# Kernel optimization log

Hardware: AMD Instinct MI355X
Metric: run time of the kernel (lower is better)

The kernel has to match this reference:

```python
import jax, jax.numpy as jnp
import numpy as np

N_NODES = 50000
N_EDGES = 800000
N_GRAPHS = 100
IN_DIM = 100
OUT_DIM = 128
N_ETYPES = 4
N_STEPS = 8


def setup_inputs() -> dict:
    key = jax.random.key(0)
    ks = jax.random.split(key, 16)
    s = 0.05
    return {
        "features": jax.random.normal(ks[0], (N_NODES, IN_DIM), jnp.float32),
        "edge_src": jax.random.randint(ks[1], (N_EDGES,), 0, N_NODES, jnp.int32),
        "edge_dst": jax.random.randint(ks[2], (N_EDGES,), 0, N_NODES, jnp.int32),
        "edge_types": jax.random.randint(ks[3], (N_EDGES,), 0, N_ETYPES, jnp.int32),
        "graph_ids": jnp.sort(jax.random.randint(ks[4], (N_NODES,), 0, N_GRAPHS, jnp.int32)),
        "W_msg": jax.random.normal(ks[5], (N_ETYPES, OUT_DIM, OUT_DIM), jnp.float32) * s,
        "b_msg": jax.random.normal(ks[6], (N_ETYPES, OUT_DIM), jnp.float32) * s,
        "W_ih": jax.random.normal(ks[7], (3 * OUT_DIM, OUT_DIM), jnp.float32) * s,
        "W_hh": jax.random.normal(ks[8], (3 * OUT_DIM, OUT_DIM), jnp.float32) * s,
        "b_ih": jax.random.normal(ks[9], (3 * OUT_DIM,), jnp.float32) * s,
        "b_hh": jax.random.normal(ks[10], (3 * OUT_DIM,), jnp.float32) * s,
        "W1": jax.random.normal(ks[11], (256, OUT_DIM), jnp.float32) * s,
        "b1": jax.random.normal(ks[12], (256,), jnp.float32) * s,
        "W2": jax.random.normal(ks[13], (1, 256), jnp.float32) * s,
        "b2": jax.random.normal(ks[14], (1,), jnp.float32) * s,
    }


def _gru_cell(x, h, W_ih, W_hh, b_ih, b_hh):
    # torch.nn.GRUCell: gate order (reset, update, new)
    gi = x @ W_ih.T + b_ih  # [N, 3D]
    gh = h @ W_hh.T + b_hh
    i_r, i_z, i_n = jnp.split(gi, 3, axis=-1)
    h_r, h_z, h_n = jnp.split(gh, 3, axis=-1)
    r = jax.nn.sigmoid(i_r + h_r)
    z = jax.nn.sigmoid(i_z + h_z)
    n = jnp.tanh(i_n + r * h_n)
    return (1.0 - z) * n + z * h


def reference(features, edge_src, edge_dst, edge_types, graph_ids,
              W_msg, b_msg, W_ih, W_hh, b_ih, b_hh, W1, b1, W2, b2):
    n_nodes = features.shape[0]
    # DGL GatedGraphConv: zero-pad input features to out_feats
    h = jnp.pad(features, ((0, 0), (0, OUT_DIM - features.shape[1])))
    for _ in range(N_STEPS):
        # per-edge-type linear transform of source features: [T, N, D]
        transformed = jnp.einsum('nd,tdf->tnf', h, W_msg) + b_msg[:, None, :]
        msgs = transformed[edge_types, edge_src]  # [E, D] gather
        a = jax.ops.segment_sum(msgs, edge_dst, num_segments=n_nodes)  # scatter-add
        h = _gru_cell(a, h, W_ih, W_hh, b_ih, b_hh)
    # masked mean pooling per graph (mask_mean over de-batchified graphs)
    counts = jax.ops.segment_sum(jnp.ones((n_nodes,), h.dtype), graph_ids,
                                 num_segments=N_GRAPHS)
    sums = jax.ops.segment_sum(h, graph_ids, num_segments=N_GRAPHS)
    pooled = sums / jnp.maximum(counts, 1.0)[:, None]  # [B, D]
    # classifier: Linear -> relu -> (dropout: eval noop) -> Linear -> sigmoid
    hidden = jax.nn.relu(pooled @ W1.T + b1)
    logits = hidden @ W2.T + b2  # [B, 1]
    return jax.nn.sigmoid(logits).squeeze(-1)  # [B]
```

## Files before the change

kernel.cpp:

```cpp
#include <hip/hip_runtime.h>
#include <hip/hip_bf16.h>
#include <math.h>

#define N_NODES 50000
#define M_PAD   50048
#define N_EDGES 800000
#define N_GRAPHS 100
#define IN_DIM 100
#define D 128
#define N_STEPS 8
#define NBINS (N_NODES * 4)
#define SCAN_BLOCKS 196

typedef unsigned short ushort_t;
typedef __bf16 bf16x8 __attribute__((ext_vector_type(8)));
typedef float f32x4 __attribute__((ext_vector_type(4)));

__device__ inline ushort_t f2b(float f) {
  __hip_bfloat16 b = __float2bfloat16(f);
  return *reinterpret_cast<ushort_t*>(&b);
}
__device__ inline float b2f(unsigned int u16) {
  unsigned int x = u16 << 16;
  return __builtin_bit_cast(float, x);
}

__device__ __attribute__((always_inline)) inline void gld16(const ushort_t* g, ushort_t* l) {
  __builtin_amdgcn_global_load_lds(
      (const __attribute__((address_space(1))) void*)g,
      (__attribute__((address_space(3))) void*)l, 16, 0, 0);
}

__global__ void pad_cast_kernel(const float* __restrict__ feat, ushort_t* __restrict__ ah) {
  int idx = blockIdx.x * blockDim.x + threadIdx.x;
  if (idx >= N_NODES * D) return;
  int n = idx >> 7, d = idx & 127;
  float v = (d < IN_DIM) ? feat[n * IN_DIM + d] : 0.0f;
  ah[(size_t)n * 256 + 128 + d] = f2b(v);
}

__global__ void prep_bts(const float* __restrict__ W_msg, ushort_t* __restrict__ BtS) {
  int idx = blockIdx.x * blockDim.x + threadIdx.x;
  if (idx >= 128 * 512) return;
  int f = idx >> 9, kp = idx & 511;
  int t = kp >> 7, k = kp & 127;
  BtS[(size_t)f * 512 + kp] = f2b(W_msg[((size_t)t * 128 + k) * 128 + f]);
}

__global__ void prep_wg(const float* __restrict__ W_ih, const float* __restrict__ W_hh,
                        const float* __restrict__ b_ih, const float* __restrict__ b_hh,
                        ushort_t* __restrict__ WgT, float* __restrict__ gbias) {
  int idx = blockIdx.x * blockDim.x + threadIdx.x;
  if (idx >= 512 * 256) return;
  int colp = idx >> 8, k = idx & 255;
  int g = colp >> 6, gate = (colp >> 4) & 3, r = colp & 15;
  int d = g * 16 + r;
  float v;
  if (gate == 3)      v = (k < 128) ? 0.f : W_hh[(size_t)(256 + d) * 128 + (k - 128)];
  else if (gate == 2) v = (k < 128) ? W_ih[(size_t)(256 + d) * 128 + k] : 0.f;
  else {
    int j0 = (gate == 0) ? d : 128 + d;
    v = (k < 128) ? W_ih[(size_t)j0 * 128 + k] : W_hh[(size_t)j0 * 128 + (k - 128)];
  }
  WgT[(size_t)colp * 256 + k] = f2b(v);
  if (k == 0) {
    float bb = (gate == 0) ? b_ih[d] + b_hh[d]
             : (gate == 1) ? b_ih[128 + d] + b_hh[128 + d]
             : (gate == 2) ? b_ih[256 + d] : b_hh[256 + d];
    gbias[colp] = bb;
  }
}

__global__ void hist_kernel(const int* __restrict__ edst, const int* __restrict__ etype,
                            int* __restrict__ cnt2, int* __restrict__ rank) {
  int e = blockIdx.x * 256 + threadIdx.x;
  if (e >= N_EDGES) return;
  rank[e] = atomicAdd(&cnt2[edst[e] * 4 + etype[e]], 1);
}

__global__ __launch_bounds__(1024) void scanA(const int* __restrict__ cnt2,
                                              int* __restrict__ tmp, int* __restrict__ bsum) {
  __shared__ int wsum[16];
  int b = blockIdx.x, t = threadIdx.x;
  int i = b * 1024 + t;
  int lane = t & 63, wid = t >> 6;
  int x = (i < NBINS) ? cnt2[i] : 0;
  #pragma unroll
  for (int s = 1; s < 64; s <<= 1) {
    int y = __shfl_up(x, s, 64);
    if (lane >= s) x += y;
  }
  if (lane == 63) wsum[wid] = x;
  __syncthreads();
  if (wid == 0) {
    int w = (lane < 16) ? wsum[lane] : 0;
    #pragma unroll
    for (int s = 1; s < 16; s <<= 1) {
      int y = __shfl_up(w, s, 64);
      if (lane >= s) w += y;
    }
    if (lane < 16) wsum[lane] = w;
  }
  __syncthreads();
  int wb = (wid > 0) ? wsum[wid - 1] : 0;
  tmp[i] = wb + x;
  if (t == 1023) bsum[b] = wsum[15];
}

__global__ __launch_bounds__(64) void scanB(const int* __restrict__ bsum,
                                            int* __restrict__ bpre) {
  int lane = threadIdx.x;
  int carry = 0;
  for (int base = 0; base < SCAN_BLOCKS; base += 64) {
    int idx = base + lane;
    int v = (idx < SCAN_BLOCKS) ? bsum[idx] : 0;
    int x = v;
    #pragma unroll
    for (int s = 1; s < 64; s <<= 1) {
      int y = __shfl_up(x, s, 64);
      if (lane >= s) x += y;
    }
    if (idx < SCAN_BLOCKS) bpre[idx] = carry + x - v;
    carry += __shfl(x, 63, 64);
  }
}

__global__ __launch_bounds__(1024) void scanC(const int* __restrict__ tmp,
                                              const int* __restrict__ bpre,
                                              int* __restrict__ offs2) {
  int b = blockIdx.x, t = threadIdx.x;
  int i = b * 1024 + t;
  if (i < NBINS) offs2[i + 1] = tmp[i] + bpre[b];
  if (i == 0) offs2[0] = 0;
}

__global__ void fill_kernel(const int* __restrict__ esrc, const int* __restrict__ edst,
                            const int* __restrict__ etype, const int* __restrict__ offs2,
                            const int* __restrict__ rank, int* __restrict__ payload) {
  int e = blockIdx.x * 256 + threadIdx.x;
  if (e >= N_EDGES) return;
  int key = edst[e] * 4 + etype[e];
  payload[offs2[key] + rank[e]] = esrc[e];
}

__global__ __launch_bounds__(256) void gather_kernel(const int* __restrict__ offs2,
    const int* __restrict__ payload, const ushort_t* __restrict__ hb,
    ushort_t* __restrict__ S, float* __restrict__ cntf) {
  int n = blockIdx.x * 4 + (threadIdx.x >> 6);
  int lane = threadIdx.x & 63;
  if (n >= N_NODES) return;
  int bb[5];
  #pragma unroll
  for (int k = 0; k < 5; ++k) bb[k] = offs2[n * 4 + k];
  float a[4][2] = {{0.f, 0.f}, {0.f, 0.f}, {0.f, 0.f}, {0.f, 0.f}};
  const ushort_t* hrow = hb + 128 + lane * 2;
  for (int base = bb[0]; base < bb[4]; base += 64) {
    int lim = min(bb[4], base + 64);
    int cnt = lim - base;
    int pe = (lane < cnt) ? payload[base + lane] : 0;
    #pragma unroll
    for (int t = 0; t < 4; ++t) {
      int lo = max(bb[t], base), hi = min(bb[t + 1], lim);
      int i = lo;
      for (; i + 4 <= hi; i += 4) {
        int s0 = __shfl(pe, i - base, 64);
        int s1 = __shfl(pe, i + 1 - base, 64);
        int s2 = __shfl(pe, i + 2 - base, 64);
        int s3 = __shfl(pe, i + 3 - base, 64);
        unsigned int u0 = *(const unsigned int*)(hrow + (size_t)s0 * 256);
        unsigned int u1 = *(const unsigned int*)(hrow + (size_t)s1 * 256);
        unsigned int u2 = *(const unsigned int*)(hrow + (size_t)s2 * 256);
        unsigned int u3 = *(const unsigned int*)(hrow + (size_t)s3 * 256);
        a[t][0] += b2f(u0 & 0xffff) + b2f(u1 & 0xffff) + b2f(u2 & 0xffff) + b2f(u3 & 0xffff);
        a[t][1] += b2f(u0 >> 16) + b2f(u1 >> 16) + b2f(u2 >> 16) + b2f(u3 >> 16);
      }
      for (; i < hi; ++i) {
        int s0 = __shfl(pe, i - base, 64);
        unsigned int u0 = *(const unsigned int*)(hrow + (size_t)s0 * 256);
        a[t][0] += b2f(u0 & 0xffff);
        a[t][1] += b2f(u0 >> 16);
      }
    }
  }
  #pragma unroll
  for (int t = 0; t < 4; ++t) {
    unsigned int packed = (unsigned int)f2b(a[t][0]) | ((unsigned int)f2b(a[t][1]) << 16);
    *(unsigned int*)(S + (size_t)n * 512 + t * 128 + lane * 2) = packed;
    if (lane == 0) cntf[n * 4 + t] = (float)(bb[t + 1] - bb[t]);
  }
}

template <int MODE, int K>
__global__ __launch_bounds__(256) void mfma_gemm(
    const ushort_t* __restrict__ A, int lda,
    const ushort_t* __restrict__ Bt,
    const float* __restrict__ bias, const float* __restrict__ b_msg,
    const float* __restrict__ cntf,
    ushort_t* __restrict__ ah_out) {
  constexpr int NT  = K / 32;
  constexpr int PRE = 3;
  constexpr int SLOT = 12288;
  __shared__ __align__(16) unsigned char smem[SLOT * 4];
  const int m0 = blockIdx.x * 64, n0 = blockIdx.y * 128;
  int tid = threadIdx.x;
  int wave = tid >> 6, lane = tid & 63;
  int wm = (wave & 1) * 32, wn = (wave >> 1) * 64;
  int quad = lane >> 4, l16 = lane & 15;

  int sr = lane >> 2, sc = lane & 3;
  const ushort_t* gA  = A  + (size_t)(m0 + wave * 16 + sr) * lda + sc * 8;
  const ushort_t* gB0 = Bt + (size_t)(n0 + wave * 32 + sr) * K   + sc * 8;
  const ushort_t* gB1 = gB0 + (size_t)16 * K;

  auto stage = [&](int slot, int t) {
    ushort_t* base = (ushort_t*)(smem + slot * SLOT);
    int k0 = t * 32;
    gld16(gA + k0,  base + wave * 512);
    gld16(gB0 + k0, base + 2048 + wave * 1024);
    gld16(gB1 + k0, base + 2048 + wave * 1024 + 512);
  };

  f32x4 acc[2][4];
  #pragma unroll
  for (int i = 0; i < 2; ++i)
    #pragma unroll
    for (int j = 0; j < 4; ++j) acc[i][j] = (f32x4){0.f, 0.f, 0.f, 0.f};

  #pragma unroll
  for (int t = 0; t < PRE; ++t) stage(t, t);

  #pragma unroll
  for (int t = 0; t < NT; ++t) {
    int infl = NT - 1 - t;
    if (infl >= 2)      asm volatile("s_waitcnt vmcnt(6) lgkmcnt(0)" ::: "memory");
    else if (infl == 1) asm volatile("s_waitcnt vmcnt(3) lgkmcnt(0)" ::: "memory");
    else                asm volatile("s_waitcnt vmcnt(0) lgkmcnt(0)" ::: "memory");
    __builtin_amdgcn_s_barrier();
    if (t + PRE < NT) stage((t + PRE) & 3, t + PRE);
    const ushort_t* As = (const ushort_t*)(smem + (t & 3) * SLOT);
    const ushort_t* Bs = As + 2048;
    bf16x8 af[2], bfr[4];
    #pragma unroll
    for (int i = 0; i < 2; ++i) af[i] = *(const bf16x8*)&As[(wm + i * 16 + l16) * 32 + quad * 8];
    #pragma unroll
    for (int j = 0; j < 4; ++j) bfr[j] = *(const bf16x8*)&Bs[(wn + j * 16 + l16) * 32 + quad * 8];
    #pragma unroll
    for (int i = 0; i < 2; ++i)
      #pragma unroll
      for (int j = 0; j < 4; ++j)
        acc[i][j] = __builtin_amdgcn_mfma_f32_16x16x32_bf16(af[i], bfr[j], acc[i][j], 0, 0, 0);
  }

  if (MODE == 2) {
    ushort_t* Ep = (ushort_t*)smem;
    float bm[4][4];
    #pragma unroll
    for (int j = 0; j < 4; ++j)
      #pragma unroll
      for (int t = 0; t < 4; ++t)
        bm[j][t] = b_msg[t * 128 + wn + j * 16 + l16];
    #pragma unroll
    for (int p = 0; p < 2; ++p) {
      if (p) __syncthreads();
      #pragma unroll
      for (int reg = 0; reg < 4; ++reg) {
        int slot = (wm >> 5) * 16 + quad * 4 + reg;
        int m = m0 + wm + p * 16 + quad * 4 + reg;
        float4 c = *(const float4*)(cntf + (size_t)m * 4);
        #pragma unroll
        for (int j = 0; j < 4; ++j) {
          float val = acc[p][j][reg] + c.x * bm[j][0] + c.y * bm[j][1]
                                     + c.z * bm[j][2] + c.w * bm[j][3];
          Ep[slot * 136 + wn + j * 16 + l16] = f2b(val);
        }
      }
      __syncthreads();
      #pragma unroll
      for (int c2 = 0; c2 < 2; ++c2) {
        int chunk = tid + 256 * c2;
        int slot = chunk >> 4, sub = chunk & 15;
        int m = m0 + (slot & 15) + (slot >> 4) * 32 + p * 16;
        *(uint4*)(ah_out + (size_t)m * 256 + sub * 8) =
            *(const uint4*)&Ep[slot * 136 + sub * 8];
      }
    }
  } else {
    ushort_t* Ap = (ushort_t*)smem;
    int db = (n0 >> 6) * 16;
    int dim_loc = (wn >> 6) * 16 + l16;
    float br = bias[n0 + wn + l16];
    float bz = bias[n0 + wn + 16 + l16];
    float bi = bias[n0 + wn + 32 + l16];
    float bh = bias[n0 + wn + 48 + l16];
    #pragma unroll
    for (int i = 0; i < 2; ++i)
      #pragma unroll
      for (int reg = 0; reg < 4; ++reg) {
        int r_loc = wm + i * 16 + quad * 4 + reg;
        int m = m0 + r_loc;
        float pr  = acc[i][0][reg] + br;
        float pz  = acc[i][1][reg] + bz;
        float in_ = acc[i][2][reg] + bi;
        float hn  = acc[i][3][reg] + bh;
        float r = 1.0f / (1.0f + expf(-pr));
        float z = 1.0f / (1.0f + expf(-pz));
        float nn = tanhf(in_ + r * hn);
        float hold = b2f(A[(size_t)m * lda + 128 + db + dim_loc]);
        float hv = (1.0f - z) * nn + z * hold;
        Ap[r_loc * 40 + dim_loc] = f2b(hv);
      }
    __syncthreads();
    {
      int row = tid >> 2, sub = tid & 3;
      *(uint4*)(ah_out + (size_t)(m0 + row) * 256 + 128 + db + sub * 8) =
          *(const uint4*)&Ap[row * 40 + sub * 8];
    }
  }
}

__global__ __launch_bounds__(128) void pool_kernel(const ushort_t* __restrict__ ah,
    const int* __restrict__ gids, float* __restrict__ pooled, float* __restrict__ gcnt) {
  __shared__ int lo_s, hi_s;
  int g = blockIdx.x, c = blockIdx.y, d = threadIdx.x;
  if (d == 0) {
    int lo = 0, hi = N_NODES;
    while (lo < hi) { int mid = (lo + hi) >> 1; if (gids[mid] < g) lo = mid + 1; else hi = mid; }
    lo_s = lo;
    int lo2 = lo, hi2 = N_NODES;
    while (lo2 < hi2) { int mid = (lo2 + hi2) >> 1; if (gids[mid] < g + 1) lo2 = mid + 1; else hi2 = mid; }
    hi_s = lo2;
  }
  __syncthreads();
  int lo = lo_s, hi = hi_s;
  int len = hi - lo;
  int b = lo + (int)(((long long)len * c) >> 3);
  int e = lo + (int)(((long long)len * (c + 1)) >> 3);
  float s = 0.f;
  for (int n = b; n < e; ++n) s += b2f(ah[(size_t)n * 256 + 128 + d]);
  if (e > b) atomicAdd(&pooled[g * 128 + d], s);
  if (c == 0 && d == 0) gcnt[g] = (float)len;
}

__global__ __launch_bounds__(256) void classifier_kernel(
    const float* __restrict__ pooled, const float* __restrict__ gcnt,
    const float* __restrict__ W1, const float* __restrict__ b1,
    const float* __restrict__ W2, const float* __restrict__ b2,
    float* __restrict__ out) {
  __shared__ float p[D];
  __shared__ float hid[256];
  __shared__ float wsum[4];
  int g = blockIdx.x;
  int t = threadIdx.x;
  float cnt = fmaxf(gcnt[g], 1.0f);
  if (t < D) p[t] = pooled[g * D + t] / cnt;
  __syncthreads();
  float acc = b1[t];
  const float* w = W1 + (size_t)t * D;
  for (int k = 0; k < D; ++k) acc += p[k] * w[k];
  hid[t] = fmaxf(acc, 0.0f);
  __syncthreads();
  float v = hid[t] * W2[t];
  for (int off = 32; off > 0; off >>= 1) v += __shfl_down(v, off, 64);
  if ((t & 63) == 0) wsum[t >> 6] = v;
  __syncthreads();
  if (t == 0) {
    float s = wsum[0] + wsum[1] + wsum[2] + wsum[3] + b2[0];
    out[g] = 1.0f / (1.0f + expf(-s));
  }
}

extern "C" void kernel_launch(void* const* d_in, const int* in_sizes, int n_in,
                              void* d_out, int out_size, void* d_ws, size_t ws_size,
                              hipStream_t stream) {
  const float* features = (const float*)d_in[0];
  const int* esrc  = (const int*)d_in[1];
  const int* edst  = (const int*)d_in[2];
  const int* etype = (const int*)d_in[3];
  const int* gids  = (const int*)d_in[4];
  const float* W_msg = (const float*)d_in[5];
  const float* b_msg = (const float*)d_in[6];
  const float* W_ih  = (const float*)d_in[7];
  const float* W_hh  = (const float*)d_in[8];
  const float* b_ih  = (const float*)d_in[9];
  const float* b_hh  = (const float*)d_in[10];
  const float* W1 = (const float*)d_in[11];
  const float* b1 = (const float*)d_in[12];
  const float* W2 = (const float*)d_in[13];
  const float* b2 = (const float*)d_in[14];
  float* out = (float*)d_out;

  char* ws = (char*)d_ws;
  size_t off_b = 0;
  auto alloc = [&](size_t bytes) -> void* {
    void* p = ws + off_b;
    off_b += (bytes + 255) & ~(size_t)255;
    return p;
  };
  ushort_t* ahA    = (ushort_t*)alloc((size_t)M_PAD * 256 * 2);
  ushort_t* ahB    = (ushort_t*)alloc((size_t)M_PAD * 256 * 2);
  ushort_t* S      = (ushort_t*)alloc((size_t)M_PAD * 512 * 2);
  float*    cntf   = (float*)alloc((size_t)M_PAD * 4 * 4);
  ushort_t* BtS    = (ushort_t*)alloc(128 * 512 * 2);
  ushort_t* WgT    = (ushort_t*)alloc(512 * 256 * 2);
  float*    gbias  = (float*)alloc(512 * 4);
  int*      cnt2   = (int*)alloc((size_t)NBINS * 4);
  int*      offs2  = (int*)alloc((size_t)(NBINS + 1) * 4);
  int*      rank   = (int*)alloc((size_t)N_EDGES * 4);
  int*      tmp    = (int*)alloc((size_t)SCAN_BLOCKS * 1024 * 4);
  int*      bsum   = (int*)alloc(SCAN_BLOCKS * 4);
  int*      bpre   = (int*)alloc(SCAN_BLOCKS * 4);
  int*      payload= (int*)alloc((size_t)N_EDGES * 4);
  float*    pooled = (float*)alloc(N_GRAPHS * 128 * 4);
  float*    gcnt   = (float*)alloc(N_GRAPHS * 4);

  pad_cast_kernel<<<(N_NODES * 128 + 255) / 256, 256, 0, stream>>>(features, ahA);
  prep_bts<<<(128 * 512 + 255) / 256, 256, 0, stream>>>(W_msg, BtS);
  prep_wg<<<(512 * 256 + 255) / 256, 256, 0, stream>>>(W_ih, W_hh, b_ih, b_hh, WgT, gbias);
  hipMemsetAsync(cnt2, 0, (size_t)NBINS * 4, stream);
  hist_kernel<<<(N_EDGES + 255) / 256, 256, 0, stream>>>(edst, etype, cnt2, rank);
  scanA<<<SCAN_BLOCKS, 1024, 0, stream>>>(cnt2, tmp, bsum);
  scanB<<<1, 64, 0, stream>>>(bsum, bpre);
  scanC<<<SCAN_BLOCKS, 1024, 0, stream>>>(tmp, bpre, offs2);
  fill_kernel<<<(N_EDGES + 255) / 256, 256, 0, stream>>>(esrc, edst, etype, offs2, rank, payload);

  ushort_t* cur = ahA;
  ushort_t* nxt = ahB;
  for (int step = 0; step < N_STEPS; ++step) {
    gather_kernel<<<(N_NODES + 3) / 4, 256, 0, stream>>>(offs2, payload, cur, S, cntf);
    mfma_gemm<2, 512><<<dim3(M_PAD / 64, 1), 256, 0, stream>>>(
        S, 512, BtS, nullptr, b_msg, cntf, cur);
    mfma_gemm<1, 256><<<dim3(M_PAD / 64, 4), 256, 0, stream>>>(
        cur, 256, WgT, gbias, nullptr, nullptr, nxt);
    ushort_t* t2 = cur; cur = nxt; nxt = t2;
  }

  hipMemsetAsync(pooled, 0, (size_t)N_GRAPHS * 128 * 4, stream);
  pool_kernel<<<dim3(N_GRAPHS, 8), 128, 0, stream>>>(cur, gids, pooled, gcnt);
  classifier_kernel<<<N_GRAPHS, 256, 0, stream>>>(pooled, gcnt, W1, b1, W2, b2, out);
}
```

Baseline: 924.0 us.

## Fuse neighbor gather with message GEMM to drop the intermediate buffer

Merges the per-node, per-edge-type gather and the message-transform GEMM into one kernel. Each 512-thread block first gathers 32 nodes' summed source features into swizzled LDS. It then runs MFMA against the message weights, which are read directly from global memory, and writes the aggregated message into the first half of the state buffer. This removes the global write and read of the large S and cntf intermediates and one launch per step. The cost is lower MFMA tile reuse and a serialized gather-then-compute phase within each block. The GRU GEMM is split out into its own non-templated kernel.

```diff
diff --git a/kernel.cpp b/kernel.cpp
--- a/kernel.cpp
+++ b/kernel.cpp
@@ -143,60 +143,122 @@
   payload[offs2[key] + rank[e]] = esrc[e];
 }
 
-__global__ __launch_bounds__(256) void gather_kernel(const int* __restrict__ offs2,
-    const int* __restrict__ payload, const ushort_t* __restrict__ hb,
-    ushort_t* __restrict__ S, float* __restrict__ cntf) {
-  int n = blockIdx.x * 4 + (threadIdx.x >> 6);
-  int lane = threadIdx.x & 63;
-  if (n >= N_NODES) return;
-  int bb[5];
-  #pragma unroll
-  for (int k = 0; k < 5; ++k) bb[k] = offs2[n * 4 + k];
-  float a[4][2] = {{0.f, 0.f}, {0.f, 0.f}, {0.f, 0.f}, {0.f, 0.f}};
+__global__ __launch_bounds__(512, 8) void fused_gather_gemm(
+    const int* __restrict__ offs2, const int* __restrict__ payload,
+    const ushort_t* __restrict__ hb,
+    const ushort_t* __restrict__ Bt,
+    const float* __restrict__ b_msg,
+    ushort_t* __restrict__ ah_out) {
+  __shared__ __align__(16) unsigned char smem[32 * 1024 + 32 * 16];
+  float* cnt_lds = (float*)(smem + 32 * 1024);
+  const int m0 = blockIdx.x * 32;
+  int tid = threadIdx.x;
+  int wave = tid >> 6, lane = tid & 63;
+
   const ushort_t* hrow = hb + 128 + lane * 2;
-  for (int base = bb[0]; base < bb[4]; base += 64) {
-    int lim = min(bb[4], base + 64);
-    int cnt = lim - base;
-    int pe = (lane < cnt) ? payload[base + lane] : 0;
+  for (int u = 0; u < 4; ++u) {
+    int nl = wave * 4 + u;
+    int n = m0 + nl;
+    int bb[5];
+    if (n < N_NODES) {
+      #pragma unroll
+      for (int k = 0; k < 5; ++k) bb[k] = offs2[n * 4 + k];
+    } else {
+      #pragma unroll
+      for (int k = 0; k < 5; ++k) bb[k] = 0;
+    }
+    float a[4][2] = {{0.f, 0.f}, {0.f, 0.f}, {0.f, 0.f}, {0.f, 0.f}};
+    for (int base = bb[0]; base < bb[4]; base += 64) {
+      int lim = min(bb[4], base + 64);
+      int cnt = lim - base;
+      int pe = (lane < cnt) ? payload[base + lane] : 0;
+      #pragma unroll
+      for (int t = 0; t < 4; ++t) {
+        int lo = max(bb[t], base), hi = min(bb[t + 1], lim);
+        int i = lo;
+        for (; i + 4 <= hi; i += 4) {
+          int s0 = __shfl(pe, i - base, 64);
+          int s1 = __shfl(pe, i + 1 - base, 64);
+          int s2 = __shfl(pe, i + 2 - base, 64);
+          int s3 = __shfl(pe, i + 3 - base, 64);
+          unsigned int u0 = *(const unsigned int*)(hrow + (size_t)s0 * 256);
+          unsigned int u1 = *(const unsigned int*)(hrow + (size_t)s1 * 256);
+          unsigned int u2 = *(const unsigned int*)(hrow + (size_t)s2 * 256);
+          unsigned int u3 = *(const unsigned int*)(hrow + (size_t)s3 * 256);
+          a[t][0] += b2f(u0 & 0xffff) + b2f(u1 & 0xffff) + b2f(u2 & 0xffff) + b2f(u3 & 0xffff);
+          a[t][1] += b2f(u0 >> 16) + b2f(u1 >> 16) + b2f(u2 >> 16) + b2f(u3 >> 16);
+        }
+        for (; i < hi; ++i) {
+          int s0 = __shfl(pe, i - base, 64);
+          unsigned int u0 = *(const unsigned int*)(hrow + (size_t)s0 * 256);
+          a[t][0] += b2f(u0 & 0xffff);
+          a[t][1] += b2f(u0 >> 16);
+        }
+      }
+    }
+    int swz = (nl & 7) << 4;
     #pragma unroll
     for (int t = 0; t < 4; ++t) {
-      int lo = max(bb[t], base), hi = min(bb[t + 1], lim);
-      int i = lo;
-      for (; i + 4 <= hi; i += 4) {
-        int s0 = __shfl(pe, i - base, 64);
-        int s1 = __shfl(pe, i + 1 - base, 64);
-        int s2 = __shfl(pe, i + 2 - base, 64);
-        int s3 = __shfl(pe, i + 3 - base, 64);
-        unsigned int u0 = *(const unsigned int*)(hrow + (size_t)s0 * 256);
-        unsigned int u1 = *(const unsigned int*)(hrow + (size_t)s1 * 256);
-        unsigned int u2 = *(const unsigned int*)(hrow + (size_t)s2 * 256);
-        unsigned int u3 = *(const unsigned int*)(hrow + (size_t)s3 * 256);
-        a[t][0] += b2f(u0 & 0xffff) + b2f(u1 & 0xffff) + b2f(u2 & 0xffff) + b2f(u3 & 0xffff);
-        a[t][1] += b2f(u0 >> 16) + b2f(u1 >> 16) + b2f(u2 >> 16) + b2f(u3 >> 16);
-      }
-      for (; i < hi; ++i) {
-        int s0 = __shfl(pe, i - base, 64);
-        unsigned int u0 = *(const unsigned int*)(hrow + (size_t)s0 * 256);
-        a[t][0] += b2f(u0 & 0xffff);
-        a[t][1] += b2f(u0 >> 16);
-      }
-    }
-  }
-  #pragma unroll
-  for (int t = 0; t < 4; ++t) {
-    unsigned int packed = (unsigned int)f2b(a[t][0]) | ((unsigned int)f2b(a[t][1]) << 16);
-    *(unsigned int*)(S + (size_t)n * 512 + t * 128 + lane * 2) = packed;
-    if (lane == 0) cntf[n * 4 + t] = (float)(bb[t + 1] - bb[t]);
-  }
-}
-
-template <int MODE, int K>
-__global__ __launch_bounds__(256) void mfma_gemm(
+      unsigned int packed = (unsigned int)f2b(a[t][0]) | ((unsigned int)f2b(a[t][1]) << 16);
+      *(unsigned int*)(smem + ((nl * 1024 + t * 256 + lane * 4) ^ swz)) = packed;
+    }
+    if (lane < 4) cnt_lds[nl * 4 + lane] = (float)(bb[lane + 1] - bb[lane]);
+  }
+  __syncthreads();
+
+  int wm = (wave & 1) * 16;
+  int wn = (wave >> 1) * 32;
+  int quad = lane >> 4, l16 = lane & 15;
+  f32x4 acc[2];
+  acc[0] = (f32x4){0.f, 0.f, 0.f, 0.f};
+  acc[1] = (f32x4){0.f, 0.f, 0.f, 0.f};
+  int arow = wm + l16;
+  int abase = arow * 1024 + quad * 16;
+  int aswz = (arow & 7) << 4;
+  const ushort_t* gB0 = Bt + (size_t)(wn + l16) * 512 + quad * 8;
+  const ushort_t* gB1 = gB0 + (size_t)16 * 512;
+  #pragma unroll 4
+  for (int k0 = 0; k0 < 512; k0 += 32) {
+    bf16x8 af = *(const bf16x8*)(smem + ((abase + k0 * 2) ^ aswz));
+    bf16x8 b0 = *(const bf16x8*)(gB0 + k0);
+    bf16x8 b1 = *(const bf16x8*)(gB1 + k0);
+    acc[0] = __builtin_amdgcn_mfma_f32_16x16x32_bf16(af, b0, acc[0], 0, 0, 0);
+    acc[1] = __builtin_amdgcn_mfma_f32_16x16x32_bf16(af, b1, acc[1], 0, 0, 0);
+  }
+  __syncthreads();
+
+  ushort_t* Ep = (ushort_t*)smem;
+  float bm[2][4];
+  #pragma unroll
+  for (int j = 0; j < 2; ++j)
+    #pragma unroll
+    for (int t = 0; t < 4; ++t)
+      bm[j][t] = b_msg[t * 128 + wn + j * 16 + l16];
+  #pragma unroll
+  for (int reg = 0; reg < 4; ++reg) {
+    int r = wm + quad * 4 + reg;
+    float4 c = *(const float4*)&cnt_lds[r * 4];
+    #pragma unroll
+    for (int j = 0; j < 2; ++j) {
+      float val = acc[j][reg] + c.x * bm[j][0] + c.y * bm[j][1]
+                              + c.z * bm[j][2] + c.w * bm[j][3];
+      Ep[r * 136 + wn + j * 16 + l16] = f2b(val);
+    }
+  }
+  __syncthreads();
+  {
+    int row = tid >> 4, sub = tid & 15;
+    *(uint4*)(ah_out + (size_t)(m0 + row) * 256 + sub * 8) =
+        *(const uint4*)&Ep[row * 136 + sub * 8];
+  }
+}
+
+__global__ __launch_bounds__(256) void mfma_gru(
     const ushort_t* __restrict__ A, int lda,
     const ushort_t* __restrict__ Bt,
-    const float* __restrict__ bias, const float* __restrict__ b_msg,
-    const float* __restrict__ cntf,
+    const float* __restrict__ bias,
     ushort_t* __restrict__ ah_out) {
+  constexpr int K = 256;
   constexpr int NT  = K / 32;
   constexpr int PRE = 3;
   constexpr int SLOT = 12288;
@@ -251,70 +313,35 @@
         acc[i][j] = __builtin_amdgcn_mfma_f32_16x16x32_bf16(af[i], bfr[j], acc[i][j], 0, 0, 0);
   }
 
-  if (MODE == 2) {
-    ushort_t* Ep = (ushort_t*)smem;
-    float bm[4][4];
-    #pragma unroll
-    for (int j = 0; j < 4; ++j)
-      #pragma unroll
-      for (int t = 0; t < 4; ++t)
-        bm[j][t] = b_msg[t * 128 + wn + j * 16 + l16];
-    #pragma unroll
-    for (int p = 0; p < 2; ++p) {
-      if (p) __syncthreads();
-      #pragma unroll
-      for (int reg = 0; reg < 4; ++reg) {
-        int slot = (wm >> 5) * 16 + quad * 4 + reg;
-        int m = m0 + wm + p * 16 + quad * 4 + reg;
-        float4 c = *(const float4*)(cntf + (size_t)m * 4);
-        #pragma unroll
-        for (int j = 0; j < 4; ++j) {
-          float val = acc[p][j][reg] + c.x * bm[j][0] + c.y * bm[j][1]
-                                     + c.z * bm[j][2] + c.w * bm[j][3];
-          Ep[slot * 136 + wn + j * 16 + l16] = f2b(val);
-        }
-      }
-      __syncthreads();
-      #pragma unroll
-      for (int c2 = 0; c2 < 2; ++c2) {
-        int chunk = tid + 256 * c2;
-        int slot = chunk >> 4, sub = chunk & 15;
-        int m = m0 + (slot & 15) + (slot >> 4) * 32 + p * 16;
-        *(uint4*)(ah_out + (size_t)m * 256 + sub * 8) =
-            *(const uint4*)&Ep[slot * 136 + sub * 8];
-      }
-    }
-  } else {
-    ushort_t* Ap = (ushort_t*)smem;
-    int db = (n0 >> 6) * 16;
-    int dim_loc = (wn >> 6) * 16 + l16;
-    float br = bias[n0 + wn + l16];
-    float bz = bias[n0 + wn + 16 + l16];
-    float bi = bias[n0 + wn + 32 + l16];
-    float bh = bias[n0 + wn + 48 + l16];
-    #pragma unroll
-    for (int i = 0; i < 2; ++i)
-      #pragma unroll
-      for (int reg = 0; reg < 4; ++reg) {
-        int r_loc = wm + i * 16 + quad * 4 + reg;
-        int m = m0 + r_loc;
-        float pr  = acc[i][0][reg] + br;
-        float pz  = acc[i][1][reg] + bz;
-        float in_ = acc[i][2][reg] + bi;
-        float hn  = acc[i][3][reg] + bh;
-        float r = 1.0f / (1.0f + expf(-pr));
-        float z = 1.0f / (1.0f + expf(-pz));
-        float nn = tanhf(in_ + r * hn);
-        float hold = b2f(A[(size_t)m * lda + 128 + db + dim_loc]);
-        float hv = (1.0f - z) * nn + z * hold;
-        Ap[r_loc * 40 + dim_loc] = f2b(hv);
-      }
-    __syncthreads();
-    {
-      int row = tid >> 2, sub = tid & 3;
-      *(uint4*)(ah_out + (size_t)(m0 + row) * 256 + 128 + db + sub * 8) =
-          *(const uint4*)&Ap[row * 40 + sub * 8];
-    }
+  ushort_t* Ap = (ushort_t*)smem;
+  int db = (n0 >> 6) * 16;
+  int dim_loc = (wn >> 6) * 16 + l16;
+  float br = bias[n0 + wn + l16];
+  float bz = bias[n0 + wn + 16 + l16];
+  float bi = bias[n0 + wn + 32 + l16];
+  float bh = bias[n0 + wn + 48 + l16];
+  #pragma unroll
+  for (int i = 0; i < 2; ++i)
+    #pragma unroll
+    for (int reg = 0; reg < 4; ++reg) {
+      int r_loc = wm + i * 16 + quad * 4 + reg;
+      int m = m0 + r_loc;
+      float pr  = acc[i][0][reg] + br;
+      float pz  = acc[i][1][reg] + bz;
+      float in_ = acc[i][2][reg] + bi;
+      float hn  = acc[i][3][reg] + bh;
+      float r = 1.0f / (1.0f + expf(-pr));
+      float z = 1.0f / (1.0f + expf(-pz));
+      float nn = tanhf(in_ + r * hn);
+      float hold = b2f(A[(size_t)m * lda + 128 + db + dim_loc]);
+      float hv = (1.0f - z) * nn + z * hold;
+      Ap[r_loc * 40 + dim_loc] = f2b(hv);
+    }
+  __syncthreads();
+  {
+    int row = tid >> 2, sub = tid & 3;
+    *(uint4*)(ah_out + (size_t)(m0 + row) * 256 + 128 + db + sub * 8) =
+        *(const uint4*)&Ap[row * 40 + sub * 8];
   }
 }
 
@@ -398,8 +425,6 @@
   };
   ushort_t* ahA    = (ushort_t*)alloc((size_t)M_PAD * 256 * 2);
   ushort_t* ahB    = (ushort_t*)alloc((size_t)M_PAD * 256 * 2);
-  ushort_t* S      = (ushort_t*)alloc((size_t)M_PAD * 512 * 2);
-  float*    cntf   = (float*)alloc((size_t)M_PAD * 4 * 4);
   ushort_t* BtS    = (ushort_t*)alloc(128 * 512 * 2);
   ushort_t* WgT    = (ushort_t*)alloc(512 * 256 * 2);
   float*    gbias  = (float*)alloc(512 * 4);
@@ -426,11 +451,10 @@
   ushort_t* cur = ahA;
   ushort_t* nxt = ahB;
   for (int step = 0; step < N_STEPS; ++step) {
-    gather_kernel<<<(N_NODES + 3) / 4, 256, 0, stream>>>(offs2, payload, cur, S, cntf);
-    mfma_gemm<2, 512><<<dim3(M_PAD / 64, 1), 256, 0, stream>>>(
-        S, 512, BtS, nullptr, b_msg, cntf, cur);
-    mfma_gemm<1, 256><<<dim3(M_PAD / 64, 4), 256, 0, stream>>>(
-        cur, 256, WgT, gbias, nullptr, nullptr, nxt);
+    fused_gather_gemm<<<M_PAD / 32, 512, 0, stream>>>(
+        offs2, payload, cur, BtS, b_msg, cur);
+    mfma_gru<<<dim3(M_PAD / 64, 4), 256, 0, stream>>>(
+        cur, 256, WgT, gbias, nxt);
     ushort_t* t2 = cur; cur = nxt; nxt = t2;
   }
 
```

New measurement: 1.139 ms. 23.3% more time.
